# Optimization experiments

Measured on AMD Instinct MI355X. Metric: run time of the kernel, lower is better.

The kernel has to match this reference:

```python
import jax, jax.numpy as jnp
import numpy as np

DELTA_V = 0.5
DELTA_D = 1.5
ALPHA = 1.0
BETA = 1.0
GAMMA = 0.001
IGNORE_LABEL = -1
MAX_VIEWS = 100
NUM_CLASSES = 19

B, D, H, W = 8, 128, 256, 256


def setup_inputs() -> dict:
    key = jax.random.key(0)
    k1, k2 = jax.random.split(key)
    feats = jax.random.normal(k1, (B, D, H, W), dtype=jnp.float32)
    labels = jax.random.randint(k2, (B, H, W), 0, NUM_CLASSES, dtype=jnp.int32)
    return {"feats": feats, "labels": labels}


def _safe_norm(sq):
    # gradient-safe sqrt: subgradient 0 at 0 (matches torch.norm at 0)
    pos = sq > 0
    return jnp.where(pos, jnp.sqrt(jnp.where(pos, sq, 1.0)), 0.0)


def reference(feats, labels):
    # feats: (B, D, H, W) -> (N, D); labels: (B, H, W) -> (N,)
    # (labels already at feats' HxW, so the nearest interpolation is identity)
    d = feats.shape[1]
    f = jnp.transpose(feats, (0, 2, 3, 1)).reshape(-1, d)
    lab = labels.reshape(-1)

    valid_pix = lab != IGNORE_LABEL
    lab0 = jnp.where(valid_pix, lab, 0)

    # per-class counts and means (vectorized replacement of the per-class loop)
    cnt = jax.ops.segment_sum(valid_pix.astype(f.dtype), lab0, num_segments=NUM_CLASSES)
    sums = jax.ops.segment_sum(jnp.where(valid_pix[:, None], f, 0.0), lab0, num_segments=NUM_CLASSES)
    safe_cnt = jnp.maximum(cnt, 1.0)
    means = sums / safe_cnt[:, None]  # (C, D)

    # class selection: present, != ignore, count > max_views
    valid_cls = cnt > MAX_VIEWS

    # --- loss_var: per-class mean of hinged distances to class mean ---
    diff = f - means[lab0]
    dist = _safe_norm(jnp.sum(diff * diff, axis=1)) - DELTA_V
    h = jnp.maximum(dist, 0.0)
    contrib = jnp.where(valid_pix & valid_cls[lab0], h * h, 0.0)
    var_c = jax.ops.segment_sum(contrib, lab0, num_segments=NUM_CLASSES) / safe_cnt
    loss_var = jnp.sum(jnp.where(valid_cls, var_c, 0.0))

    # --- loss_reg: sum of norms of class means ---
    mean_norm = _safe_norm(jnp.sum(means * means, axis=1))
    loss_reg = jnp.sum(jnp.where(valid_cls, mean_norm, 0.0))

    # --- loss_dist: faithful to the original (buggy) double loop:
    # a ranges over all T valid classes (sorted by id); b ranges over the first
    # T-1 valid classes of cluster_mean_lst, including b == a.
    cls_ids = jnp.arange(NUM_CLASSES)
    last_valid = jnp.max(jnp.where(valid_cls, cls_ids, -1))
    bmask = valid_cls & (cls_ids != last_valid)
    pd = means[:, None, :] - means[None, :, :]  # (C, C, D) -- C is tiny
    pdn = _safe_norm(jnp.sum(pd * pd, axis=-1))
    hd = jnp.maximum(2.0 * DELTA_D - pdn, 0.0)
    mask2 = valid_cls[:, None] & bmask[None, :]
    loss_dist = jnp.sum(jnp.where(mask2, hd * hd, 0.0))

    t = jnp.sum(valid_cls).astype(f.dtype)
    loss = (ALPHA * loss_var / t
            + BETA * loss_dist / (t * (t - 1.0))
            + GAMMA * loss_reg / t)
    return loss
```

## Files before the change

kernel.cpp:

```cpp
#include <hip/hip_runtime.h>

#define C 19
#define DCH 128
#define HWSZ 65536
#define TPB 256

#define WS_SUMS  0
#define WS_CNT   2432
#define WS_VAR   2451
#define WS_MEANS 2560
#define WS_VALID 4992
#define WS_SCAL  5011
#define WS_ZERO_END 2470

__global__ void k0_init(float* __restrict__ ws) {
    int i = blockIdx.x * blockDim.x + threadIdx.x;
    if (i < WS_ZERO_END) ws[i] = 0.f;
}

#define K1_NB  1024
#define K1_RPX 4096

__global__ __launch_bounds__(TPB) void k1_sums(const float* __restrict__ feats,
                                               const int* __restrict__ labels,
                                               float* __restrict__ ws) {
    __shared__ int llab[K1_RPX];

    const int t = threadIdx.x;
    const int lane = t & 63;
    const int w = t >> 6;
    const int bid = blockIdx.x;
    const int b  = bid >> 7;
    const int r  = (bid >> 3) & 15;
    const int dg = bid & 7;

    const int* lb = labels + b * HWSZ + r * K1_RPX;
    int4 myl[4];
#pragma unroll
    for (int u = 0; u < 4; ++u) {
        int4 v = *reinterpret_cast<const int4*>(lb + (u * TPB + t) * 4);
        myl[u] = v;
        *reinterpret_cast<int4*>(&llab[(u * TPB + t) * 4]) = v;
    }
    __syncthreads();

    if (dg == 0) {
        float cr[C];
#pragma unroll
        for (int c = 0; c < C; ++c) cr[c] = 0.f;
#pragma unroll
        for (int u = 0; u < 4; ++u) {
#pragma unroll
            for (int c = 0; c < C; ++c) {
                cr[c] += (myl[u].x == c ? 1.f : 0.f);
                cr[c] += (myl[u].y == c ? 1.f : 0.f);
                cr[c] += (myl[u].z == c ? 1.f : 0.f);
                cr[c] += (myl[u].w == c ? 1.f : 0.f);
            }
        }
#pragma unroll
        for (int c = 0; c < C; ++c)
            for (int m = 1; m < 64; m <<= 1) cr[c] += __shfl_xor(cr[c], m);
        float v = cr[0];
#pragma unroll
        for (int c = 1; c < C; ++c) v = (lane == c) ? cr[c] : v;
        if (lane < C) atomicAdd(&ws[WS_CNT + lane], v);
    }

    const int dbase = dg * 16 + w * 4;
    const float* fp0 = feats + (((size_t)(b * DCH + dbase + 0)) << 16) + r * K1_RPX;
    const float* fp1 = feats + (((size_t)(b * DCH + dbase + 1)) << 16) + r * K1_RPX;
    const float* fp2 = feats + (((size_t)(b * DCH + dbase + 2)) << 16) + r * K1_RPX;
    const float* fp3 = feats + (((size_t)(b * DCH + dbase + 3)) << 16) + r * K1_RPX;

    float acc[4][C];
#pragma unroll
    for (int p = 0; p < 4; ++p)
#pragma unroll
        for (int c = 0; c < C; ++c) acc[p][c] = 0.f;

#pragma unroll 1
    for (int jb = 0; jb < 16; ++jb) {
        const int off = jb * 256 + lane * 4;
        float4 x0 = *reinterpret_cast<const float4*>(fp0 + off);
        float4 x1 = *reinterpret_cast<const float4*>(fp1 + off);
        float4 x2 = *reinterpret_cast<const float4*>(fp2 + off);
        float4 x3 = *reinterpret_cast<const float4*>(fp3 + off);
        int4 l = *reinterpret_cast<const int4*>(&llab[(jb * 64 + lane) * 4]);
#pragma unroll
        for (int c = 0; c < C; ++c) {
            const float ohx = (l.x == c) ? 1.f : 0.f;
            const float ohy = (l.y == c) ? 1.f : 0.f;
            const float ohz = (l.z == c) ? 1.f : 0.f;
            const float ohw = (l.w == c) ? 1.f : 0.f;
            acc[0][c] = fmaf(ohx, x0.x, acc[0][c]);
            acc[0][c] = fmaf(ohy, x0.y, acc[0][c]);
            acc[0][c] = fmaf(ohz, x0.z, acc[0][c]);
            acc[0][c] = fmaf(ohw, x0.w, acc[0][c]);
            acc[1][c] = fmaf(ohx, x1.x, acc[1][c]);
            acc[1][c] = fmaf(ohy, x1.y, acc[1][c]);
            acc[1][c] = fmaf(ohz, x1.z, acc[1][c]);
            acc[1][c] = fmaf(ohw, x1.w, acc[1][c]);
            acc[2][c] = fmaf(ohx, x2.x, acc[2][c]);
            acc[2][c] = fmaf(ohy, x2.y, acc[2][c]);
            acc[2][c] = fmaf(ohz, x2.z, acc[2][c]);
            acc[2][c] = fmaf(ohw, x2.w, acc[2][c]);
            acc[3][c] = fmaf(ohx, x3.x, acc[3][c]);
            acc[3][c] = fmaf(ohy, x3.y, acc[3][c]);
            acc[3][c] = fmaf(ohz, x3.z, acc[3][c]);
            acc[3][c] = fmaf(ohw, x3.w, acc[3][c]);
        }
    }

#pragma unroll
    for (int p = 0; p < 4; ++p) {
#pragma unroll
        for (int c = 0; c < C; ++c)
            for (int m = 1; m < 64; m <<= 1) acc[p][c] += __shfl_xor(acc[p][c], m);
        float v = acc[p][0];
#pragma unroll
        for (int c = 1; c < C; ++c) v = (lane == c) ? acc[p][c] : v;
        if (lane < C) atomicAdd(&ws[WS_SUMS + (dbase + p) * C + lane], v);
    }
}

__global__ __launch_bounds__(TPB) void k2_means(float* __restrict__ ws) {
    __shared__ float lm[DCH * C];
    __shared__ float lcnt[C];
    __shared__ float lvalid[C];
    __shared__ float lreg;
    __shared__ float ldist;
    __shared__ int   llast;
    __shared__ float ltv;
    int t = threadIdx.x;
    if (t == 0) { lreg = 0.f; ldist = 0.f; }
    if (t < C) {
        float c = ws[WS_CNT + t];
        lcnt[t] = c;
        lvalid[t] = (c > 100.f) ? 1.f : 0.f;
    }
    __syncthreads();
    for (int i = t; i < DCH * C; i += TPB) {
        int c = i % C;
        float m = ws[WS_SUMS + i] / fmaxf(lcnt[c], 1.f);
        lm[i] = m;
        ws[WS_MEANS + i] = m;
    }
    if (t == 0) {
        float tv = 0.f; int last = -1;
        for (int c2 = 0; c2 < C; ++c2) if (lvalid[c2] > 0.5f) { tv += 1.f; last = c2; }
        ltv = tv; llast = last;
    }
    __syncthreads();
    if (t < C) {
        float s = 0.f;
        for (int d = 0; d < DCH; ++d) { float m = lm[d * C + t]; s += m * m; }
        float nrm = (s > 0.f) ? sqrtf(s) : 0.f;
        if (lvalid[t] > 0.5f) atomicAdd(&lreg, nrm);
    }
    for (int pr = t; pr < C * C; pr += TPB) {
        int a = pr / C, b2 = pr % C;
        if (lvalid[a] > 0.5f && lvalid[b2] > 0.5f && b2 != llast) {
            float s = 0.f;
            for (int d = 0; d < DCH; ++d) {
                float df = lm[d * C + a] - lm[d * C + b2];
                s += df * df;
            }
            float nrm = (s > 0.f) ? sqrtf(s) : 0.f;
            float hd = fmaxf(3.0f - nrm, 0.f);
            atomicAdd(&ldist, hd * hd);
        }
    }
    __syncthreads();
    if (t < C) ws[WS_VALID + t] = lvalid[t];
    if (t == 0) {
        ws[WS_SCAL + 0] = lreg;
        ws[WS_SCAL + 1] = ldist;
        ws[WS_SCAL + 2] = ltv;
    }
}

#define K3_NB 2048
#define MPAD 20

__global__ __launch_bounds__(TPB) void k3_var(const float* __restrict__ feats,
                                              const int* __restrict__ labels,
                                              float* __restrict__ ws) {
    __shared__ float lmS[DCH * MPAD];
    __shared__ float lvalid[C];
    __shared__ float lvar[C];
    const int t = threadIdx.x;
    for (int i = t; i < DCH * C; i += TPB) {
        int d = i / C, c = i - d * C;
        lmS[d * MPAD + c] = ws[WS_MEANS + i];
    }
    if (t < C) { lvalid[t] = ws[WS_VALID + t]; lvar[t] = 0.f; }
    __syncthreads();

    const int qloc = t >> 2;
    const int k = t & 3;
    const int q = blockIdx.x * 64 + qloc;
    const int b = q >> 14;
    const int p = (q & 16383) * 4;

    const int4 lab4 = *reinterpret_cast<const int4*>(labels + b * HWSZ + p);
    const int l0 = lab4.x < 0 ? 0 : lab4.x;
    const int l1 = lab4.y < 0 ? 0 : lab4.y;
    const int l2 = lab4.z < 0 ? 0 : lab4.z;
    const int l3 = lab4.w < 0 ? 0 : lab4.w;

    const float* fb = feats + (((size_t)(b * DCH + k * 32)) << 16) + p;
    float a0 = 0.f, a1 = 0.f, a2 = 0.f, a3 = 0.f;
    for (int i = 0; i < 32; i += 8) {
        float4 xb[8];
#pragma unroll
        for (int u = 0; u < 8; ++u)
            xb[u] = *reinterpret_cast<const float4*>(fb + ((size_t)(i + u) << 16));
#pragma unroll
        for (int u = 0; u < 8; ++u) {
            const float* mr = &lmS[(k * 32 + i + u) * MPAD];
            float d0 = xb[u].x - mr[l0]; a0 = fmaf(d0, d0, a0);
            float d1 = xb[u].y - mr[l1]; a1 = fmaf(d1, d1, a1);
            float d2 = xb[u].z - mr[l2]; a2 = fmaf(d2, d2, a2);
            float d3 = xb[u].w - mr[l3]; a3 = fmaf(d3, d3, a3);
        }
    }
    a0 += __shfl_xor(a0, 1); a0 += __shfl_xor(a0, 2);
    a1 += __shfl_xor(a1, 1); a1 += __shfl_xor(a1, 2);
    a2 += __shfl_xor(a2, 1); a2 += __shfl_xor(a2, 2);
    a3 += __shfl_xor(a3, 1); a3 += __shfl_xor(a3, 2);

    if (k == 0) {
        auto hinge2 = [&](float a, int rawlab, int l) -> float {
            float nrm = (a > 0.f) ? sqrtf(a) : 0.f;
            float h = fmaxf(nrm - 0.5f, 0.f);
            float v = h * h;
            return (rawlab >= 0 && lvalid[l] > 0.5f) ? v : 0.f;
        };
        atomicAdd(&lvar[l0], hinge2(a0, lab4.x, l0));
        atomicAdd(&lvar[l1], hinge2(a1, lab4.y, l1));
        atomicAdd(&lvar[l2], hinge2(a2, lab4.z, l2));
        atomicAdd(&lvar[l3], hinge2(a3, lab4.w, l3));
    }
    __syncthreads();
    if (t < C) atomicAdd(&ws[WS_VAR + t], lvar[t]);
}

__global__ void k4_final(const float* __restrict__ ws, float* __restrict__ out) {
    if (threadIdx.x == 0) {
        float loss_var = 0.f;
        for (int c = 0; c < C; ++c) {
            float cnt = ws[WS_CNT + c];
            float v = ws[WS_VAR + c] / fmaxf(cnt, 1.f);
            if (ws[WS_VALID + c] > 0.5f) loss_var += v;
        }
        float reg  = ws[WS_SCAL + 0];
        float dist = ws[WS_SCAL + 1];
        float tv   = ws[WS_SCAL + 2];
        float loss = loss_var / tv + dist / (tv * (tv - 1.0f)) + 0.001f * reg / tv;
        out[0] = loss;
    }
}

extern "C" void kernel_launch(void* const* d_in, const int* in_sizes, int n_in,
                              void* d_out, int out_size, void* d_ws, size_t ws_size,
                              hipStream_t stream) {
    const float* feats  = (const float*)d_in[0];
    const int*   labels = (const int*)d_in[1];
    float* ws  = (float*)d_ws;
    float* out = (float*)d_out;

    hipLaunchKernelGGL(k0_init,  dim3((WS_ZERO_END + 255) / 256), dim3(256), 0, stream, ws);
    hipLaunchKernelGGL(k1_sums,  dim3(K1_NB), dim3(TPB), 0, stream, feats, labels, ws);
    hipLaunchKernelGGL(k2_means, dim3(1),   dim3(TPB), 0, stream, ws);
    hipLaunchKernelGGL(k3_var,   dim3(K3_NB), dim3(TPB), 0, stream, feats, labels, ws);
    hipLaunchKernelGGL(k4_final, dim3(1),   dim3(64),  0, stream, ws, out);
}
```

Before: 442.4 us.

## Fold tiny means and final kernels into last-block tails via ticket counters

Removes the single-block k2_means and k4_final launches by having the last-finishing block of k1_sums and k3_var, detected with an atomic ticket counter, do that work. The init kernel is replaced by hipMemsetAsync, which also zeroes the two new ticket counters. This cuts launch count and inter-kernel gaps, but adds a fence and atomic per block and serializes the tail work onto one block. Shared memory in k1 is unioned to hold the means scratch.

```diff
diff --git a/kernel.cpp b/kernel.cpp
--- a/kernel.cpp
+++ b/kernel.cpp
@@ -8,15 +8,14 @@
 #define WS_SUMS  0
 #define WS_CNT   2432
 #define WS_VAR   2451
+#define WS_TKT1  2470
+#define WS_TKT2  2471
+#define WS_ZERO_END 2472
 #define WS_MEANS 2560
 #define WS_VALID 4992
 #define WS_SCAL  5011
-#define WS_ZERO_END 2470
-
-__global__ void k0_init(float* __restrict__ ws) {
-    int i = blockIdx.x * blockDim.x + threadIdx.x;
-    if (i < WS_ZERO_END) ws[i] = 0.f;
-}
+
+#define AGENT_LOAD(p) __hip_atomic_load((p), __ATOMIC_RELAXED, __HIP_MEMORY_SCOPE_AGENT)
 
 #define K1_NB  1024
 #define K1_RPX 4096
@@ -24,7 +23,17 @@
 __global__ __launch_bounds__(TPB) void k1_sums(const float* __restrict__ feats,
                                                const int* __restrict__ labels,
                                                float* __restrict__ ws) {
-    __shared__ int llab[K1_RPX];
+    __shared__ union {
+        int llab[K1_RPX];
+        struct {
+            float lm[DCH * C];
+            float lcnt[C];
+            float lvalid[C];
+            float lreg, ldist, ltv;
+            int   llast;
+        } p2;
+    } sh;
+    __shared__ int is_last;
 
     const int t = threadIdx.x;
     const int lane = t & 63;
@@ -40,7 +49,7 @@
     for (int u = 0; u < 4; ++u) {
         int4 v = *reinterpret_cast<const int4*>(lb + (u * TPB + t) * 4);
         myl[u] = v;
-        *reinterpret_cast<int4*>(&llab[(u * TPB + t) * 4]) = v;
+        *reinterpret_cast<int4*>(&sh.llab[(u * TPB + t) * 4]) = v;
     }
     __syncthreads();
 
@@ -86,7 +95,7 @@
         float4 x1 = *reinterpret_cast<const float4*>(fp1 + off);
         float4 x2 = *reinterpret_cast<const float4*>(fp2 + off);
         float4 x3 = *reinterpret_cast<const float4*>(fp3 + off);
-        int4 l = *reinterpret_cast<const int4*>(&llab[(jb * 64 + lane) * 4]);
+        int4 l = *reinterpret_cast<const int4*>(&sh.llab[(jb * 64 + lane) * 4]);
 #pragma unroll
         for (int c = 0; c < C; ++c) {
             const float ohx = (l.x == c) ? 1.f : 0.f;
@@ -122,61 +131,62 @@
         for (int c = 1; c < C; ++c) v = (lane == c) ? acc[p][c] : v;
         if (lane < C) atomicAdd(&ws[WS_SUMS + (dbase + p) * C + lane], v);
     }
-}
-
-__global__ __launch_bounds__(TPB) void k2_means(float* __restrict__ ws) {
-    __shared__ float lm[DCH * C];
-    __shared__ float lcnt[C];
-    __shared__ float lvalid[C];
-    __shared__ float lreg;
-    __shared__ float ldist;
-    __shared__ int   llast;
-    __shared__ float ltv;
-    int t = threadIdx.x;
-    if (t == 0) { lreg = 0.f; ldist = 0.f; }
+
+    __threadfence();
+    if (t == 0) {
+        unsigned tk = __hip_atomic_fetch_add(
+            reinterpret_cast<unsigned*>(ws) + WS_TKT1, 1u,
+            __ATOMIC_ACQ_REL, __HIP_MEMORY_SCOPE_AGENT);
+        is_last = (tk == K1_NB - 1);
+    }
+    __syncthreads();
+    if (!is_last) return;
+    __threadfence();
+
+    if (t == 0) { sh.p2.lreg = 0.f; sh.p2.ldist = 0.f; }
     if (t < C) {
-        float c = ws[WS_CNT + t];
-        lcnt[t] = c;
-        lvalid[t] = (c > 100.f) ? 1.f : 0.f;
+        float c = AGENT_LOAD(&ws[WS_CNT + t]);
+        sh.p2.lcnt[t] = c;
+        sh.p2.lvalid[t] = (c > 100.f) ? 1.f : 0.f;
     }
     __syncthreads();
     for (int i = t; i < DCH * C; i += TPB) {
         int c = i % C;
-        float m = ws[WS_SUMS + i] / fmaxf(lcnt[c], 1.f);
-        lm[i] = m;
+        float m = AGENT_LOAD(&ws[WS_SUMS + i]) / fmaxf(sh.p2.lcnt[c], 1.f);
+        sh.p2.lm[i] = m;
         ws[WS_MEANS + i] = m;
     }
     if (t == 0) {
         float tv = 0.f; int last = -1;
-        for (int c2 = 0; c2 < C; ++c2) if (lvalid[c2] > 0.5f) { tv += 1.f; last = c2; }
-        ltv = tv; llast = last;
+        for (int c2 = 0; c2 < C; ++c2) if (sh.p2.lvalid[c2] > 0.5f) { tv += 1.f; last = c2; }
+        sh.p2.ltv = tv; sh.p2.llast = last;
     }
     __syncthreads();
     if (t < C) {
         float s = 0.f;
-        for (int d = 0; d < DCH; ++d) { float m = lm[d * C + t]; s += m * m; }
+        for (int d = 0; d < DCH; ++d) { float m = sh.p2.lm[d * C + t]; s += m * m; }
         float nrm = (s > 0.f) ? sqrtf(s) : 0.f;
-        if (lvalid[t] > 0.5f) atomicAdd(&lreg, nrm);
+        if (sh.p2.lvalid[t] > 0.5f) atomicAdd(&sh.p2.lreg, nrm);
     }
     for (int pr = t; pr < C * C; pr += TPB) {
         int a = pr / C, b2 = pr % C;
-        if (lvalid[a] > 0.5f && lvalid[b2] > 0.5f && b2 != llast) {
+        if (sh.p2.lvalid[a] > 0.5f && sh.p2.lvalid[b2] > 0.5f && b2 != sh.p2.llast) {
             float s = 0.f;
             for (int d = 0; d < DCH; ++d) {
-                float df = lm[d * C + a] - lm[d * C + b2];
+                float df = sh.p2.lm[d * C + a] - sh.p2.lm[d * C + b2];
                 s += df * df;
             }
             float nrm = (s > 0.f) ? sqrtf(s) : 0.f;
             float hd = fmaxf(3.0f - nrm, 0.f);
-            atomicAdd(&ldist, hd * hd);
-        }
-    }
-    __syncthreads();
-    if (t < C) ws[WS_VALID + t] = lvalid[t];
-    if (t == 0) {
-        ws[WS_SCAL + 0] = lreg;
-        ws[WS_SCAL + 1] = ldist;
-        ws[WS_SCAL + 2] = ltv;
+            atomicAdd(&sh.p2.ldist, hd * hd);
+        }
+    }
+    __syncthreads();
+    if (t < C) ws[WS_VALID + t] = sh.p2.lvalid[t];
+    if (t == 0) {
+        ws[WS_SCAL + 0] = sh.p2.lreg;
+        ws[WS_SCAL + 1] = sh.p2.ldist;
+        ws[WS_SCAL + 2] = sh.p2.ltv;
     }
 }
 
@@ -185,10 +195,12 @@
 
 __global__ __launch_bounds__(TPB) void k3_var(const float* __restrict__ feats,
                                               const int* __restrict__ labels,
-                                              float* __restrict__ ws) {
+                                              float* __restrict__ ws,
+                                              float* __restrict__ out) {
     __shared__ float lmS[DCH * MPAD];
     __shared__ float lvalid[C];
     __shared__ float lvar[C];
+    __shared__ int is_last;
     const int t = threadIdx.x;
     for (int i = t; i < DCH * C; i += TPB) {
         int d = i / C, c = i - d * C;
@@ -244,14 +256,23 @@
     }
     __syncthreads();
     if (t < C) atomicAdd(&ws[WS_VAR + t], lvar[t]);
-}
-
-__global__ void k4_final(const float* __restrict__ ws, float* __restrict__ out) {
-    if (threadIdx.x == 0) {
+
+    __threadfence();
+    if (t == 0) {
+        unsigned tk = __hip_atomic_fetch_add(
+            reinterpret_cast<unsigned*>(ws) + WS_TKT2, 1u,
+            __ATOMIC_ACQ_REL, __HIP_MEMORY_SCOPE_AGENT);
+        is_last = (tk == K3_NB - 1);
+    }
+    __syncthreads();
+    if (!is_last) return;
+
+    if (t == 0) {
+        __threadfence();
         float loss_var = 0.f;
         for (int c = 0; c < C; ++c) {
-            float cnt = ws[WS_CNT + c];
-            float v = ws[WS_VAR + c] / fmaxf(cnt, 1.f);
+            float cnt = AGENT_LOAD(&ws[WS_CNT + c]);
+            float v = AGENT_LOAD(&ws[WS_VAR + c]) / fmaxf(cnt, 1.f);
             if (ws[WS_VALID + c] > 0.5f) loss_var += v;
         }
         float reg  = ws[WS_SCAL + 0];
@@ -270,9 +291,7 @@
     float* ws  = (float*)d_ws;
     float* out = (float*)d_out;
 
-    hipLaunchKernelGGL(k0_init,  dim3((WS_ZERO_END + 255) / 256), dim3(256), 0, stream, ws);
-    hipLaunchKernelGGL(k1_sums,  dim3(K1_NB), dim3(TPB), 0, stream, feats, labels, ws);
-    hipLaunchKernelGGL(k2_means, dim3(1),   dim3(TPB), 0, stream, ws);
-    hipLaunchKernelGGL(k3_var,   dim3(K3_NB), dim3(TPB), 0, stream, feats, labels, ws);
-    hipLaunchKernelGGL(k4_final, dim3(1),   dim3(64),  0, stream, ws, out);
+    hipMemsetAsync(ws, 0, WS_ZERO_END * sizeof(float), stream);
+    hipLaunchKernelGGL(k1_sums, dim3(K1_NB), dim3(TPB), 0, stream, feats, labels, ws);
+    hipLaunchKernelGGL(k3_var,  dim3(K3_NB), dim3(TPB), 0, stream, feats, labels, ws, out);
 }
```

After: 861.9 us. 1.95x slower.
